# Kernel tuning notes

Measured on AMD Instinct MI355X. Metric: run time of the kernel, lower is better.

## Reference

```python
import jax, jax.numpy as jnp
import numpy as np

N, M, K = 32768, 16, 64
HALF_LOG_2PI = 0.9189385332046727  # 0.5*log(2*pi)
EPS = 2.220446049250313e-16       # np.finfo(np.float64).eps, as in original


def setup_inputs() -> dict:
    key = jax.random.key(0)
    k1, k2, k3 = jax.random.split(key, 3)
    X = jax.random.normal(k1, (N, M), dtype=jnp.float32)
    wk0_logits = jnp.ones((1, K), dtype=jnp.float32)
    W_logits = jnp.ones((M, K, K), dtype=jnp.float32)
    mu = jax.random.uniform(k2, (M, K, K), dtype=jnp.float32, minval=-4.0, maxval=4.0)
    pre_sigma = jax.random.uniform(k3, (M, K, K), dtype=jnp.float32, minval=0.0, maxval=5.0)
    return {"X": X, "wk0_logits": wk0_logits, "W_logits": W_logits,
            "mu": mu, "pre_sigma": pre_sigma}


def reference(X, wk0_logits, W_logits, mu, pre_sigma):
    n, k = X.shape[0], wk0_logits.shape[1]
    wk0 = jax.nn.softmax(wk0_logits, axis=1)[0]          # (K,)
    # tf softmax(W_logits[i], axis=0) == softmax over axis=1 of (M,K,K)
    logW = jax.nn.log_softmax(W_logits, axis=1)          # (M,K,K)
    sigma = jax.nn.softplus(pre_sigma)                   # (M,K,K)

    prod0 = jnp.broadcast_to(jnp.eye(k, dtype=X.dtype), (n, k, k))

    def step(prod, inputs):
        x, lw, m, s = inputs                             # x:(N,), lw/m/s:(K,K)
        # Normal(mu, sigma).log_prob(x)
        z = (x[:, None, None] - m) / s                   # (N,K,K)
        logp = -0.5 * jnp.square(z) - jnp.log(s) - HALF_LOG_2PI
        result = jnp.exp(lw + logp)                      # (N,K,K)
        # prod @ result^T per sample
        new_prod = jnp.einsum('nij,nkj->nik', prod, result)
        return new_prod, None

    prod, _ = jax.lax.scan(step, prod0, (X.T, logW, mu, sigma))
    # squeeze(wk0 @ prod) summed over last axis -> (N,)
    likelihoods = jnp.einsum('k,nkj->n', wk0, prod)
    return jnp.log(likelihoods + EPS)
```

## Files before the change

kernel.cpp:

```cpp
#include <hip/hip_runtime.h>
#include <math.h>


#define TTG_N 32768
#define TTG_M 16
#define TTG_K 64

typedef float f32x2 __attribute__((ext_vector_type(2)));

static constexpr float kHalfLog2Pi = 0.9189385332046727f;
static constexpr float kEps        = 2.220446049250313e-16f;
static constexpr float kLog2e      = 1.4426950408889634f;

#if defined(__has_builtin)
#if __has_builtin(__builtin_amdgcn_exp2f)
#define TTG_EXP2(x) __builtin_amdgcn_exp2f(x)
#else
#define TTG_EXP2(x) exp2f(x)
#endif
#else
#define TTG_EXP2(x) exp2f(x)
#endif

#define PK_SEL0(d, s0, xx, s2)                                                \
  asm("v_pk_fma_f32 %0, %1, %2, %3 op_sel:[0,0,0] op_sel_hi:[1,0,1]"          \
      : "=v"(d) : "v"(s0), "v"(xx), "v"(s2))
#define PK_SEL1(d, s0, xx, s2)                                                \
  asm("v_pk_fma_f32 %0, %1, %2, %3 op_sel:[0,1,0] op_sel_hi:[1,1,1]"          \
      : "=v"(d) : "v"(s0), "v"(xx), "v"(s2))

__global__ void ttg_prep_wk0(const float* __restrict__ logits,
                             float* __restrict__ wk0) {
  int i = threadIdx.x;
  float l = logits[i];
  float mx = l;
  for (int d = 1; d < 64; d <<= 1) mx = fmaxf(mx, __shfl_xor(mx, d));
  float e = expf(l - mx);
  float s = e;
  for (int d = 1; d < 64; d <<= 1) s += __shfl_xor(s, d);
  wk0[i] = e / s;
}

__global__ void ttg_prep_params(const float* __restrict__ W,
                                const float* __restrict__ mu,
                                const float* __restrict__ ps,
                                float* __restrict__ P) {
  int b = blockIdx.x;
  int m = b >> 6;
  int j = b & 63;
  int i = threadIdx.x;
  int idx = (m * TTG_K + i) * TTG_K + j;

  float w = W[idx];
  float mx = w;
  for (int d = 1; d < 64; d <<= 1) mx = fmaxf(mx, __shfl_xor(mx, d));
  float e = expf(w - mx);
  float s = e;
  for (int d = 1; d < 64; d <<= 1) s += __shfl_xor(s, d);
  float lw = w - mx - logf(s);

  float mv  = mu[idx];
  float sig = log1pf(expf(ps[idx]));
  float inv2 = 1.0f / (sig * sig);
  float A = -0.5f * inv2 * kLog2e;
  float B = mv * inv2 * kLog2e;
  float C = (lw - logf(sig) - kHalfLog2Pi - 0.5f * mv * mv * inv2) * kLog2e;

  float* base = P + (size_t)m * 12288;
  int pi = ((j >> 1) * TTG_K + i) * 2 + (j & 1);
  base[pi]        = A;
  base[4096 + pi] = B;
  base[8192 + pi] = C;
}

__global__ __launch_bounds__(512, 4) void ttg_main(
    const float* __restrict__ X, const float* __restrict__ P,
    const float* __restrict__ wk0, float* __restrict__ out) {
  __shared__ __align__(16) float prA[TTG_K * TTG_K];
  __shared__ __align__(16) float prB[TTG_K * TTG_K];
  __shared__ __align__(16) float prC[TTG_K * TTG_K];
  __shared__ __align__(16) float ub[64 * TTG_K];
  __shared__ __align__(16) float xbT[TTG_M * 64];

  const int tid  = threadIdx.x;
  const int lane = tid & 63;
  const int wv   = __builtin_amdgcn_readfirstlane(tid >> 6);
  const int blk  = blockIdx.x;

  if (tid < 256) {
    float4 v = ((const float4*)X)[blk * 256 + tid];
    int s = tid >> 2, f0 = (tid & 3) * 4;
    xbT[(f0 + 0) * 64 + s] = v.x;
    xbT[(f0 + 1) * 64 + s] = v.y;
    xbT[(f0 + 2) * 64 + s] = v.z;
    xbT[(f0 + 3) * 64 + s] = v.w;
  }
#pragma unroll
  for (int r = 0; r < 8; ++r) {
    int idx = tid + r * 512;
    ub[idx] = wk0[idx & 63];
  }
  {
    const float4* src = (const float4*)P;
#pragma unroll
    for (int r = 0; r < 2; ++r) ((float4*)prA)[tid + r * 512] = src[tid + r * 512];
#pragma unroll
    for (int r = 0; r < 2; ++r) ((float4*)prB)[tid + r * 512] = src[1024 + tid + r * 512];
#pragma unroll
    for (int r = 0; r < 2; ++r) ((float4*)prC)[tid + r * 512] = src[2048 + tid + r * 512];
  }
  __syncthreads();

  float a0, a1, a2s, a3, a4, a5, a6, a7;
  for (int m = 0; m < TTG_M; ++m) {
    float4 pf0, pf1, pf2, pf3, pf4, pf5;
    if (m < TTG_M - 1) {
      const float4* src = (const float4*)(P + (size_t)(m + 1) * 12288);
      pf0 = src[tid];
      pf1 = src[tid + 512];
      pf2 = src[tid + 1024];
      pf3 = src[tid + 1536];
      pf4 = src[tid + 2048];
      pf5 = src[tid + 2560];
    }
    const f32x2* xrow = (const f32x2*)(xbT + m * 64 + wv * 8);
    const f32x2 xx01 = xrow[0], xx23 = xrow[1], xx45 = xrow[2], xx67 = xrow[3];

    f32x2 acc0 = {0.f, 0.f}, acc1 = acc0, acc2 = acc0, acc3 = acc0;
    f32x2 acc4 = acc0, acc5 = acc0, acc6 = acc0, acc7 = acc0;
    const f32x2* pA = ((const f32x2*)prA) + lane;
    const f32x2* pB = ((const f32x2*)prB) + lane;
    const f32x2* pC = ((const f32x2*)prC) + lane;
    const f32x2* pU = (const f32x2*)(ub + wv * 8 * TTG_K);

#define TTG_SAMPLE(SEL, XX, UROW, ACC)                                        \
    {                                                                         \
      const f32x2 u2 = pU[(UROW) * 32 + j2];                                  \
      f32x2 h, t;                                                             \
      SEL(h, a2, XX, b2);                                                     \
      SEL(t, h, XX, c2);                                                      \
      f32x2 e2 = {TTG_EXP2(t[0]), TTG_EXP2(t[1])};                            \
      ACC += e2 * u2;                                                         \
    }

#pragma unroll 2
    for (int j2 = 0; j2 < 32; ++j2) {
      const f32x2 a2 = pA[j2 * 64];
      const f32x2 b2 = pB[j2 * 64];
      const f32x2 c2 = pC[j2 * 64];
      TTG_SAMPLE(PK_SEL0, xx01, 0, acc0)
      TTG_SAMPLE(PK_SEL1, xx01, 1, acc1)
      TTG_SAMPLE(PK_SEL0, xx23, 2, acc2)
      TTG_SAMPLE(PK_SEL1, xx23, 3, acc3)
      TTG_SAMPLE(PK_SEL0, xx45, 4, acc4)
      TTG_SAMPLE(PK_SEL1, xx45, 5, acc5)
      TTG_SAMPLE(PK_SEL0, xx67, 6, acc6)
      TTG_SAMPLE(PK_SEL1, xx67, 7, acc7)
    }
#undef TTG_SAMPLE

    a0 = acc0[0] + acc0[1];
    a1 = acc1[0] + acc1[1];
    a2s = acc2[0] + acc2[1];
    a3 = acc3[0] + acc3[1];
    a4 = acc4[0] + acc4[1];
    a5 = acc5[0] + acc5[1];
    a6 = acc6[0] + acc6[1];
    a7 = acc7[0] + acc7[1];

    if (m < TTG_M - 1) {
      __syncthreads();
      float* ud = ub + wv * 8 * TTG_K + lane;
      ud[0 * TTG_K] = a0;
      ud[1 * TTG_K] = a1;
      ud[2 * TTG_K] = a2s;
      ud[3 * TTG_K] = a3;
      ud[4 * TTG_K] = a4;
      ud[5 * TTG_K] = a5;
      ud[6 * TTG_K] = a6;
      ud[7 * TTG_K] = a7;
      ((float4*)prA)[tid]       = pf0;
      ((float4*)prA)[tid + 512] = pf1;
      ((float4*)prB)[tid]       = pf2;
      ((float4*)prB)[tid + 512] = pf3;
      ((float4*)prC)[tid]       = pf4;
      ((float4*)prC)[tid + 512] = pf5;
      __syncthreads();
    }
  }

  float r[8] = {a0, a1, a2s, a3, a4, a5, a6, a7};
#pragma unroll
  for (int c = 0; c < 8; ++c) {
#pragma unroll
    for (int d = 1; d < 64; d <<= 1) r[c] += __shfl_xor(r[c], d);
  }
  if (lane == 0) {
    const int s0 = blk * 64 + wv * 8;
#pragma unroll
    for (int c = 0; c < 8; ++c) out[s0 + c] = logf(r[c] + kEps);
  }
}

extern "C" void kernel_launch(void* const* d_in, const int* in_sizes, int n_in,
                              void* d_out, int out_size, void* d_ws, size_t ws_size,
                              hipStream_t stream) {
  const float* X   = (const float*)d_in[0];
  const float* wl  = (const float*)d_in[1];
  const float* W   = (const float*)d_in[2];
  const float* mu  = (const float*)d_in[3];
  const float* ps  = (const float*)d_in[4];
  float* out = (float*)d_out;

  float* wk0 = (float*)d_ws;
  float* P   = wk0 + 256;

  ttg_prep_wk0<<<1, 64, 0, stream>>>(wl, wk0);
  ttg_prep_params<<<TTG_M * TTG_K, 64, 0, stream>>>(W, mu, ps, P);
  ttg_main<<<TTG_N / 64, 512, 0, stream>>>(X, P, wk0, out);
}
```

Baseline: 272.0 us.

## Use 1024-thread blocks with 4 samples per wave and compiler packed FMAs

Measured after the change: 267.2 us. No clear change (-1.8%).

```diff
diff --git a/kernel.cpp b/kernel.cpp
--- a/kernel.cpp
+++ b/kernel.cpp
@@ -21,13 +21,6 @@
 #else
 #define TTG_EXP2(x) exp2f(x)
 #endif
-
-#define PK_SEL0(d, s0, xx, s2)                                                \
-  asm("v_pk_fma_f32 %0, %1, %2, %3 op_sel:[0,0,0] op_sel_hi:[1,0,1]"          \
-      : "=v"(d) : "v"(s0), "v"(xx), "v"(s2))
-#define PK_SEL1(d, s0, xx, s2)                                                \
-  asm("v_pk_fma_f32 %0, %1, %2, %3 op_sel:[0,1,0] op_sel_hi:[1,1,1]"          \
-      : "=v"(d) : "v"(s0), "v"(xx), "v"(s2))
 
 __global__ void ttg_prep_wk0(const float* __restrict__ logits,
                              float* __restrict__ wk0) {
@@ -73,7 +66,7 @@
   base[8192 + pi] = C;
 }
 
-__global__ __launch_bounds__(512, 4) void ttg_main(
+__global__ __launch_bounds__(1024, 8) void ttg_main(
     const float* __restrict__ X, const float* __restrict__ P,
     const float* __restrict__ wk0, float* __restrict__ out) {
   __shared__ __align__(16) float prA[TTG_K * TTG_K];
@@ -96,109 +89,85 @@
     xbT[(f0 + 3) * 64 + s] = v.w;
   }
 #pragma unroll
-  for (int r = 0; r < 8; ++r) {
-    int idx = tid + r * 512;
+  for (int r = 0; r < 4; ++r) {
+    int idx = tid + r * 1024;
     ub[idx] = wk0[idx & 63];
   }
   {
     const float4* src = (const float4*)P;
-#pragma unroll
-    for (int r = 0; r < 2; ++r) ((float4*)prA)[tid + r * 512] = src[tid + r * 512];
-#pragma unroll
-    for (int r = 0; r < 2; ++r) ((float4*)prB)[tid + r * 512] = src[1024 + tid + r * 512];
-#pragma unroll
-    for (int r = 0; r < 2; ++r) ((float4*)prC)[tid + r * 512] = src[2048 + tid + r * 512];
+    ((float4*)prA)[tid] = src[tid];
+    ((float4*)prB)[tid] = src[1024 + tid];
+    ((float4*)prC)[tid] = src[2048 + tid];
   }
   __syncthreads();
 
-  float a0, a1, a2s, a3, a4, a5, a6, a7;
+  float aL0, aL1, aL2, aL3, aH0, aH1, aH2, aH3;
   for (int m = 0; m < TTG_M; ++m) {
-    float4 pf0, pf1, pf2, pf3, pf4, pf5;
+    float4 pf0, pf1, pf2;
     if (m < TTG_M - 1) {
       const float4* src = (const float4*)(P + (size_t)(m + 1) * 12288);
       pf0 = src[tid];
-      pf1 = src[tid + 512];
-      pf2 = src[tid + 1024];
-      pf3 = src[tid + 1536];
-      pf4 = src[tid + 2048];
-      pf5 = src[tid + 2560];
+      pf1 = src[tid + 1024];
+      pf2 = src[tid + 2048];
     }
-    const f32x2* xrow = (const f32x2*)(xbT + m * 64 + wv * 8);
-    const f32x2 xx01 = xrow[0], xx23 = xrow[1], xx45 = xrow[2], xx67 = xrow[3];
+    const float* xr = xbT + m * 64 + wv * 4;
+    const f32x2 xs0 = {xr[0], xr[0]};
+    const f32x2 xs1 = {xr[1], xr[1]};
+    const f32x2 xs2 = {xr[2], xr[2]};
+    const f32x2 xs3 = {xr[3], xr[3]};
 
-    f32x2 acc0 = {0.f, 0.f}, acc1 = acc0, acc2 = acc0, acc3 = acc0;
-    f32x2 acc4 = acc0, acc5 = acc0, acc6 = acc0, acc7 = acc0;
+    aL0 = aL1 = aL2 = aL3 = 0.f;
+    aH0 = aH1 = aH2 = aH3 = 0.f;
     const f32x2* pA = ((const f32x2*)prA) + lane;
     const f32x2* pB = ((const f32x2*)prB) + lane;
     const f32x2* pC = ((const f32x2*)prC) + lane;
-    const f32x2* pU = (const f32x2*)(ub + wv * 8 * TTG_K);
+    const f32x2* pU = (const f32x2*)(ub + wv * 4 * TTG_K);
 
-#define TTG_SAMPLE(SEL, XX, UROW, ACC)                                        \
+#define TTG_SAMPLE(XS, UROW, AL, AH)                                          \
     {                                                                         \
       const f32x2 u2 = pU[(UROW) * 32 + j2];                                  \
-      f32x2 h, t;                                                             \
-      SEL(h, a2, XX, b2);                                                     \
-      SEL(t, h, XX, c2);                                                      \
-      f32x2 e2 = {TTG_EXP2(t[0]), TTG_EXP2(t[1])};                            \
-      ACC += e2 * u2;                                                         \
+      f32x2 h = __builtin_elementwise_fma(a2, XS, b2);                        \
+      f32x2 t = __builtin_elementwise_fma(h, XS, c2);                         \
+      AL = fmaf(TTG_EXP2(t[0]), u2[0], AL);                                   \
+      AH = fmaf(TTG_EXP2(t[1]), u2[1], AH);                                   \
     }
 
-#pragma unroll 2
+#pragma unroll
     for (int j2 = 0; j2 < 32; ++j2) {
       const f32x2 a2 = pA[j2 * 64];
       const f32x2 b2 = pB[j2 * 64];
       const f32x2 c2 = pC[j2 * 64];
-      TTG_SAMPLE(PK_SEL0, xx01, 0, acc0)
-      TTG_SAMPLE(PK_SEL1, xx01, 1, acc1)
-      TTG_SAMPLE(PK_SEL0, xx23, 2, acc2)
-      TTG_SAMPLE(PK_SEL1, xx23, 3, acc3)
-      TTG_SAMPLE(PK_SEL0, xx45, 4, acc4)
-      TTG_SAMPLE(PK_SEL1, xx45, 5, acc5)
-      TTG_SAMPLE(PK_SEL0, xx67, 6, acc6)
-      TTG_SAMPLE(PK_SEL1, xx67, 7, acc7)
+      TTG_SAMPLE(xs0, 0, aL0, aH0)
+      TTG_SAMPLE(xs1, 1, aL1, aH1)
+      TTG_SAMPLE(xs2, 2, aL2, aH2)
+      TTG_SAMPLE(xs3, 3, aL3, aH3)
     }
 #undef TTG_SAMPLE
 
-    a0 = acc0[0] + acc0[1];
-    a1 = acc1[0] + acc1[1];
-    a2s = acc2[0] + acc2[1];
-    a3 = acc3[0] + acc3[1];
-    a4 = acc4[0] + acc4[1];
-    a5 = acc5[0] + acc5[1];
-    a6 = acc6[0] + acc6[1];
-    a7 = acc7[0] + acc7[1];
-
     if (m < TTG_M - 1) {
       __syncthreads();
-      float* ud = ub + wv * 8 * TTG_K + lane;
-      ud[0 * TTG_K] = a0;
-      ud[1 * TTG_K] = a1;
-      ud[2 * TTG_K] = a2s;
-      ud[3 * TTG_K] = a3;
-      ud[4 * TTG_K] = a4;
-      ud[5 * TTG_K] = a5;
-      ud[6 * TTG_K] = a6;
-      ud[7 * TTG_K] = a7;
-      ((float4*)prA)[tid]       = pf0;
-      ((float4*)prA)[tid + 512] = pf1;
-      ((float4*)prB)[tid]       = pf2;
-      ((float4*)prB)[tid + 512] = pf3;
-      ((float4*)prC)[tid]       = pf4;
-      ((float4*)prC)[tid + 512] = pf5;
+      float* ud = ub + wv * 4 * TTG_K + lane;
+      ud[0 * TTG_K] = aL0 + aH0;
+      ud[1 * TTG_K] = aL1 + aH1;
+      ud[2 * TTG_K] = aL2 + aH2;
+      ud[3 * TTG_K] = aL3 + aH3;
+      ((float4*)prA)[tid] = pf0;
+      ((float4*)prB)[tid] = pf1;
+      ((float4*)prC)[tid] = pf2;
       __syncthreads();
     }
   }
 
-  float r[8] = {a0, a1, a2s, a3, a4, a5, a6, a7};
+  float r[4] = {aL0 + aH0, aL1 + aH1, aL2 + aH2, aL3 + aH3};
 #pragma unroll
-  for (int c = 0; c < 8; ++c) {
+  for (int c = 0; c < 4; ++c) {
 #pragma unroll
     for (int d = 1; d < 64; d <<= 1) r[c] += __shfl_xor(r[c], d);
   }
   if (lane == 0) {
-    const int s0 = blk * 64 + wv * 8;
+    const int s0 = blk * 64 + wv * 4;
 #pragma unroll
-    for (int c = 0; c < 8; ++c) out[s0 + c] = logf(r[c] + kEps);
+    for (int c = 0; c < 4; ++c) out[s0 + c] = logf(r[c] + kEps);
   }
 }
 
@@ -217,5 +186,5 @@
 
   ttg_prep_wk0<<<1, 64, 0, stream>>>(wl, wk0);
   ttg_prep_params<<<TTG_M * TTG_K, 64, 0, stream>>>(W, mu, ps, P);
-  ttg_main<<<TTG_N / 64, 512, 0, stream>>>(X, P, wk0, out);
+  ttg_main<<<TTG_N / 64, 1024, 0, stream>>>(X, P, wk0, out);
 }
```
